# Kernel tuning notes

Measured on AMD Instinct MI355X. Metric: run time of the kernel, lower is better.

## Reference

```python
import jax, jax.numpy as jnp
import numpy as np
import math

B, T, C = 4, 2048, 768
H = 12
D = C // H  # head dim 64

def setup_inputs() -> dict:
    key = jax.random.key(0)
    ks = jax.random.split(key, 7)
    hidden_states = jax.random.normal(ks[0], (B, T, C), dtype=jnp.float32)
    attention_mask = jnp.ones((B, T), dtype=jnp.float32)
    # torch nn.Linear weights are [out, in]; y = x @ W.T + b
    s = 1.0 / math.sqrt(C)
    Wq = jax.random.uniform(ks[1], (C, C), jnp.float32, -s, s)
    bq = jax.random.uniform(ks[2], (C,), jnp.float32, -s, s)
    Wk = jax.random.uniform(ks[3], (C, C), jnp.float32, -s, s)
    bk = jax.random.uniform(ks[4], (C,), jnp.float32, -s, s)
    Wv = jax.random.uniform(ks[5], (C, C), jnp.float32, -s, s)
    bv = jax.random.uniform(ks[6], (C,), jnp.float32, -s, s)
    return {"hidden_states": hidden_states, "attention_mask": attention_mask,
            "Wq": Wq, "bq": bq, "Wk": Wk, "bk": bk, "Wv": Wv, "bv": bv}

def _split_heads(x):
    # [B,T,C] -> [B,H,T,D]
    b, t, c = x.shape
    return x.reshape(b, t, H, D).transpose(0, 2, 1, 3)

def reference(hidden_states, attention_mask, Wq, bq, Wk, bk, Wv, bv):
    q = _split_heads(hidden_states @ Wq.T + bq)
    k = _split_heads(hidden_states @ Wk.T + bk)
    v = _split_heads(hidden_states @ Wv.T + bv)
    scores = jnp.einsum("bhqd,bhkd->bhqk", q, k) / jnp.sqrt(jnp.float32(D))
    # mask: [B,T] -> additive bias [B,1,1,T]
    bias = (1.0 - attention_mask)[:, None, None, :] * -10000.0
    scores = scores + bias
    probs = jax.nn.softmax(scores, axis=-1)  # dropout prob = 0 -> identity
    ctx = jnp.einsum("bhqk,bhkd->bhqd", probs, v)
    # [B,H,T,D] -> [B,T,C]
    return ctx.transpose(0, 2, 1, 3).reshape(hidden_states.shape[0], hidden_states.shape[1], C)
```

## Files before the change

### kernel.cpp

```cpp
#include <hip/hip_runtime.h>
#include <hip/hip_bf16.h>
#include <cstdint>

#define DI __device__ __forceinline__

constexpr int Bz = 4, Tz = 2048, Cz = 768, Hz = 12, Dz = 64;
constexpr float QSCALE = 0.18033688011112042f;

typedef __attribute__((ext_vector_type(4))) float f32x4;
typedef __attribute__((ext_vector_type(16))) float f32x16;
typedef __attribute__((ext_vector_type(8))) __bf16 bf16x8;
typedef __attribute__((ext_vector_type(4))) __bf16 bf16x4;
typedef __attribute__((ext_vector_type(2))) __bf16 bf16x2;

typedef __attribute__((address_space(1))) void gvoid;
typedef __attribute__((address_space(3))) void lvoid;

DI void gload16(const void* g, void* l) {
  __builtin_amdgcn_global_load_lds((gvoid*)g, (lvoid*)l, 16, 0, 0);
}

DI f32x4 mfma16(bf16x8 a, bf16x8 b, f32x4 c) {
  return __builtin_amdgcn_mfma_f32_16x16x32_bf16(a, b, c, 0, 0, 0);
}
DI f32x16 mfma32(bf16x8 a, bf16x8 b, f32x16 c) {
  return __builtin_amdgcn_mfma_f32_32x32x16_bf16(a, b, c, 0, 0, 0);
}

DI uint32_t pk2(float a, float b) {
  bf16x2 t;
  t[0] = (__bf16)a;
  t[1] = (__bf16)b;
  return __builtin_bit_cast(uint32_t, t);
}

union FragU { bf16x8 v; uint32_t u[4]; };

__global__ void cvt_f32_bf16_k(const float* __restrict__ src,
                               __bf16* __restrict__ dst, int n4) {
  int i = blockIdx.x * blockDim.x + threadIdx.x;
  if (i >= n4) return;
  const float4 v = reinterpret_cast<const float4*>(src)[i];
  bf16x4 r = {(__bf16)v.x, (__bf16)v.y, (__bf16)v.z, (__bf16)v.w};
  reinterpret_cast<bf16x4*>(dst)[i] = r;
}

__global__ void cvt_w3_k(const float* __restrict__ wq, const float* __restrict__ wk,
                         const float* __restrict__ wv, __bf16* __restrict__ dst) {
  int i = blockIdx.x * blockDim.x + threadIdx.x;
  const int which = i / 147456;
  const int r = i - which * 147456;
  const float* s = (which == 0) ? wq : (which == 1) ? wk : wv;
  const float4 v = reinterpret_cast<const float4*>(s)[r];
  bf16x4 o = {(__bf16)v.x, (__bf16)v.y, (__bf16)v.z, (__bf16)v.w};
  reinterpret_cast<bf16x4*>(dst)[i] = o;
}

__global__ __launch_bounds__(256, 4) void qkv_gemm_k(
    const __bf16* __restrict__ Xb, const __bf16* __restrict__ Wb,
    const float* __restrict__ bq, const float* __restrict__ bk,
    const float* __restrict__ bv, __bf16* __restrict__ Qo,
    __bf16* __restrict__ Ko, __bf16* __restrict__ Vo) {
  __shared__ __align__(16) __bf16 As[128 * 64];
  __shared__ __align__(16) __bf16 Bs[128 * 64];

  const int tid = threadIdx.x;
  const int lane = tid & 63;
  const int w = tid >> 6;
  const int wr = w >> 1, wc = w & 1;
  const int g = lane >> 4, lr = lane & 15;

  const int wgid = (blockIdx.x & 7) * 144 + (blockIdx.x >> 3);
  const int tn = wgid % 18, tm = wgid / 18;
  const int m0 = tm * 128, n0 = tn * 128;

  f32x4 acc[4][4] = {};

  for (int kt = 0; kt < Cz; kt += 64) {
#pragma unroll
    for (int rep = 0; rep < 4; ++rep) {
      const int c = rep * 256 + tid;
      const int row = c >> 3, blk = c & 7;
      const int col = ((blk ^ (row & 7)) << 3);
      gload16(&Xb[(size_t)(m0 + row) * Cz + kt + col], &As[c << 3]);
      gload16(&Wb[(size_t)(n0 + row) * Cz + kt + col], &Bs[c << 3]);
    }
    __syncthreads();
#pragma unroll
    for (int kk = 0; kk < 2; ++kk) {
      bf16x8 a[4], b[4];
#pragma unroll
      for (int m = 0; m < 4; ++m) {
        const int row = wr * 64 + m * 16 + lr;
        a[m] = *reinterpret_cast<const bf16x8*>(
            &As[row * 64 + (((kk * 4 + g) ^ (row & 7)) << 3)]);
      }
#pragma unroll
      for (int n = 0; n < 4; ++n) {
        const int row = wc * 64 + n * 16 + lr;
        b[n] = *reinterpret_cast<const bf16x8*>(
            &Bs[row * 64 + (((kk * 4 + g) ^ (row & 7)) << 3)]);
      }
      __builtin_amdgcn_s_setprio(1);
#pragma unroll
      for (int m = 0; m < 4; ++m)
#pragma unroll
        for (int n = 0; n < 4; ++n) acc[m][n] = mfma16(a[m], b[n], acc[m][n]);
      __builtin_amdgcn_s_setprio(0);
    }
    __syncthreads();
  }

#pragma unroll
  for (int n = 0; n < 4; ++n) {
    const int gn = n0 + wc * 64 + n * 16 + lr;
    const int which = gn / Cz;
    const int cc = gn - which * Cz;
    const int h = cc >> 6, d = cc & 63;
    const float* bsrc = (which == 0) ? bq : (which == 1) ? bk : bv;
    const float bsv = bsrc[cc];
    __bf16* dst = (which == 0) ? Qo : (which == 1) ? Ko : Vo;
#pragma unroll
    for (int m = 0; m < 4; ++m) {
#pragma unroll
      for (int j = 0; j < 4; ++j) {
        const int gm = m0 + wr * 64 + m * 16 + g * 4 + j;
        const int bb = gm >> 11, t = gm & 2047;
        const int bh = bb * Hz + h;
        float v = acc[m][n][j] + bsv;
        if (which == 0) v *= QSCALE;
        const size_t idx = (which == 2) ? ((size_t)(bh * Dz + d) * Tz + t)
                                        : ((size_t)(bh * Tz + t) * Dz + d);
        dst[idx] = (__bf16)v;
      }
    }
  }
}

__global__ __launch_bounds__(256, 3) void attn_k(
    const __bf16* __restrict__ Qg, const __bf16* __restrict__ Kg,
    const __bf16* __restrict__ Vg, const float* __restrict__ mask,
    float* __restrict__ out) {
  __shared__ __align__(16) __bf16 Ks[2][4096];
  __shared__ __align__(16) __bf16 Vs[2][4096];

  const int tid = threadIdx.x;
  const int lane = tid & 63;
  const int w = tid >> 6;
  const int hi = lane >> 5;
  const int l31 = lane & 31;

  const int wg = (blockIdx.x & 7) * 96 + (blockIdx.x >> 3);
  const int bh = wg >> 4, qt = wg & 15;
  const int bb = bh / Hz, h = bh - bb * Hz;
  const int q0 = qt * 128 + w * 32;

  const size_t qkbase = (size_t)bh * Tz * Dz;
  const size_t vbase = (size_t)bh * Dz * Tz;
  const float* maskp = &mask[bb * Tz];

  int* flag = (int*)&Ks[1][0];
  if (tid == 0) *flag = 0;
  __syncthreads();
  {
    int mybad = 0;
    for (int i = tid; i < Tz; i += 256) mybad |= (maskp[i] != 1.0f);
    if (__any(mybad) && lane == 0) atomicOr(flag, 1);
  }

#pragma unroll
  for (int rep = 0; rep < 2; ++rep) {
    const int c = rep * 256 + tid;
    const int row = c >> 3, blk = c & 7;
    const int col = ((blk ^ (row & 7)) << 3);
    gload16(&Kg[qkbase + (size_t)row * Dz + col], &Ks[0][c << 3]);
    gload16(&Vg[vbase + (size_t)row * Tz + col], &Vs[0][c << 3]);
  }

  bf16x8 qB[4];
#pragma unroll
  for (int ks = 0; ks < 4; ++ks)
    qB[ks] = *reinterpret_cast<const bf16x8*>(
        &Qg[qkbase + (size_t)(q0 + l31) * Dz + ks * 16 + hi * 8]);

  __syncthreads();
  const bool use_mask = (*flag != 0);

  int rOff[4];
#pragma unroll
  for (int i = 0; i < 4; ++i)
    rOff[i] = l31 * 64 + (((i * 2 + hi) ^ (l31 & 7)) << 3);

  f32x16 o0 = {}, o1 = {};
  float lpart = 0.f;

  for (int t2 = 0; t2 < 16; ++t2) {
#pragma unroll
    for (int sub = 0; sub < 2; ++sub) {
      const int t = 2 * t2 + sub;
      __syncthreads();
      if (t < 31) {
        const int kt1 = (t + 1) * 64;
#pragma unroll
        for (int rep = 0; rep < 2; ++rep) {
          const int c = rep * 256 + tid;
          const int row = c >> 3, blk = c & 7;
          const int col = ((blk ^ (row & 7)) << 3);
          gload16(&Kg[qkbase + (size_t)(kt1 + row) * Dz + col],
                  &Ks[sub ^ 1][c << 3]);
          gload16(&Vg[vbase + (size_t)row * Tz + kt1 + col],
                  &Vs[sub ^ 1][c << 3]);
        }
      }
      const int kt = t * 64;

#pragma unroll
      for (int kblk = 0; kblk < 2; ++kblk) {
        bf16x8 kA[4], vB0[2], vB1[2];
#pragma unroll
        for (int ks = 0; ks < 4; ++ks)
          kA[ks] = *reinterpret_cast<const bf16x8*>(
              &Ks[sub][kblk * 2048 + rOff[ks]]);
#pragma unroll
        for (int pss = 0; pss < 2; ++pss) {
          vB0[pss] = *reinterpret_cast<const bf16x8*>(
              &Vs[sub][rOff[kblk * 2 + pss]]);
          vB1[pss] = *reinterpret_cast<const bf16x8*>(
              &Vs[sub][2048 + rOff[kblk * 2 + pss]]);
        }

        f32x16 s = {};
        __builtin_amdgcn_s_setprio(1);
#pragma unroll
        for (int ks = 0; ks < 4; ++ks) s = mfma32(kA[ks], qB[ks], s);
        __builtin_amdgcn_s_setprio(0);

        float p[16];
        if (use_mask) {
#pragma unroll
          for (int r = 0; r < 16; ++r) {
            const int kg = kt + kblk * 32 + (r & 3) + 8 * (r >> 2) + 4 * hi;
            p[r] = __builtin_amdgcn_exp2f(
                s[r] + (1.0f - maskp[kg]) * -14426.950408889634f);
            lpart += p[r];
          }
        } else {
#pragma unroll
          for (int r = 0; r < 16; ++r) {
            p[r] = __builtin_amdgcn_exp2f(s[r]);
            lpart += p[r];
          }
        }

        uint32_t a0 = pk2(p[0], p[1]), a1 = pk2(p[4], p[5]);
        uint32_t a2 = pk2(p[8], p[9]), a3 = pk2(p[12], p[13]);
        uint32_t b0 = pk2(p[2], p[3]), b1 = pk2(p[6], p[7]);
        uint32_t b2 = pk2(p[10], p[11]), b3 = pk2(p[14], p[15]);
        asm volatile("v_permlane32_swap_b32 %0, %1" : "+v"(a0), "+v"(a1));
        asm volatile("v_permlane32_swap_b32 %0, %1" : "+v"(b0), "+v"(b1));
        asm volatile("v_permlane32_swap_b32 %0, %1" : "+v"(a2), "+v"(a3));
        asm volatile("v_permlane32_swap_b32 %0, %1" : "+v"(b2), "+v"(b3));
        FragU pf0, pf1;
        pf0.u[0] = a0; pf0.u[1] = b0; pf0.u[2] = a1; pf0.u[3] = b1;
        pf1.u[0] = a2; pf1.u[1] = b2; pf1.u[2] = a3; pf1.u[3] = b3;

        __builtin_amdgcn_s_setprio(1);
        o0 = mfma32(pf0.v, vB0[0], o0);
        o1 = mfma32(pf0.v, vB1[0], o1);
        o0 = mfma32(pf1.v, vB0[1], o0);
        o1 = mfma32(pf1.v, vB1[1], o1);
        __builtin_amdgcn_s_setprio(0);
      }
    }
  }

  float lfin = lpart + __shfl_xor(lpart, 32);
  const float inv = 1.0f / lfin;
#pragma unroll
  for (int r = 0; r < 16; ++r) {
    const int qr = (r & 3) + 8 * (r >> 2) + 4 * hi;
    const float invr = __shfl(inv, qr);
    float* orow = &out[(size_t)(bb * Tz + q0 + qr) * Cz + h * Dz + l31];
    orow[0] = o0[r] * invr;
    orow[32] = o1[r] * invr;
  }
}

extern "C" void kernel_launch(void* const* d_in, const int* in_sizes, int n_in,
                              void* d_out, int out_size, void* d_ws,
                              size_t ws_size, hipStream_t stream) {
  const float* x = (const float*)d_in[0];
  const float* mask = (const float*)d_in[1];
  const float* Wq = (const float*)d_in[2];
  const float* bq = (const float*)d_in[3];
  const float* Wk = (const float*)d_in[4];
  const float* bk = (const float*)d_in[5];
  const float* Wv = (const float*)d_in[6];
  const float* bv = (const float*)d_in[7];
  float* out = (float*)d_out;

  char* ws = (char*)d_ws;
  __bf16* Xb = (__bf16*)ws;
  __bf16* Wb = (__bf16*)(ws + 12582912);
  __bf16* Qb = (__bf16*)(ws + 16131072);
  __bf16* Kb = (__bf16*)(ws + 16131072 + 12582912);
  __bf16* Vb = (__bf16*)(ws + 16131072 + 2 * 12582912);

  cvt_f32_bf16_k<<<6144, 256, 0, stream>>>(x, Xb, 1572864);
  cvt_w3_k<<<1728, 256, 0, stream>>>(Wq, Wk, Wv, Wb);
  qkv_gemm_k<<<1152, 256, 0, stream>>>(Xb, Wb, bq, bk, bv, Qb, Kb, Vb);
  attn_k<<<768, 256, 0, stream>>>(Qb, Kb, Vb, mask, out);
}
```

Baseline: 135.5 us.

## Store V in MFMA-fragment layout and load it directly into registers

The QKV GEMM epilogue now writes V in a chunked layout that matches the MFMA B-fragment order, using packed 4-element stores. The attention kernel then reads V fragments straight from global memory into registers, with no LDS staging, and drops the V shared-memory buffers. This is meant to cut LDS traffic and footprint and to vectorize the V stores. The two conversion kernels are also merged into one launch. In exchange, V loads are now synchronous global reads at the top of each tile, which may expose latency because there is no prefetch. The converter also keeps a dead duplicate assignment.

```diff
diff --git a/kernel.cpp b/kernel.cpp
--- a/kernel.cpp
+++ b/kernel.cpp
@@ -36,24 +36,27 @@
 
 union FragU { bf16x8 v; uint32_t u[4]; };
 
-__global__ void cvt_f32_bf16_k(const float* __restrict__ src,
-                               __bf16* __restrict__ dst, int n4) {
+__global__ void cvt_all_k(const float* __restrict__ x,
+                          const float* __restrict__ wq, const float* __restrict__ wk,
+                          const float* __restrict__ wv, __bf16* __restrict__ Xb,
+                          __bf16* __restrict__ Wb) {
   int i = blockIdx.x * blockDim.x + threadIdx.x;
-  if (i >= n4) return;
-  const float4 v = reinterpret_cast<const float4*>(src)[i];
-  bf16x4 r = {(__bf16)v.x, (__bf16)v.y, (__bf16)v.z, (__bf16)v.w};
-  reinterpret_cast<bf16x4*>(dst)[i] = r;
-}
-
-__global__ void cvt_w3_k(const float* __restrict__ wq, const float* __restrict__ wk,
-                         const float* __restrict__ wv, __bf16* __restrict__ dst) {
-  int i = blockIdx.x * blockDim.x + threadIdx.x;
-  const int which = i / 147456;
-  const int r = i - which * 147456;
-  const float* s = (which == 0) ? wq : (which == 1) ? wk : wv;
+  const float* s;
+  __bf16* d;
+  int r;
+  if (i < 1572864) {
+    s = x; d = Xb; r = i;
+  } else {
+    int j = i - 1572864;
+    const int which = j / 147456;
+    r = j - which * 147456;
+    s = (which == 0) ? wq : (which == 1) ? wk : wv;
+    d = Wb + which * 589824 * 2;
+    d = Wb + which * 589824;
+  }
   const float4 v = reinterpret_cast<const float4*>(s)[r];
   bf16x4 o = {(__bf16)v.x, (__bf16)v.y, (__bf16)v.z, (__bf16)v.w};
-  reinterpret_cast<bf16x4*>(dst)[i] = o;
+  reinterpret_cast<bf16x4*>(d)[r] = o;
 }
 
 __global__ __launch_bounds__(256, 4) void qkv_gemm_k(
@@ -111,27 +114,45 @@
     __syncthreads();
   }
 
-#pragma unroll
-  for (int n = 0; n < 4; ++n) {
-    const int gn = n0 + wc * 64 + n * 16 + lr;
-    const int which = gn / Cz;
-    const int cc = gn - which * Cz;
-    const int h = cc >> 6, d = cc & 63;
-    const float* bsrc = (which == 0) ? bq : (which == 1) ? bk : bv;
-    const float bsv = bsrc[cc];
-    __bf16* dst = (which == 0) ? Qo : (which == 1) ? Ko : Vo;
-#pragma unroll
-    for (int m = 0; m < 4; ++m) {
-#pragma unroll
-      for (int j = 0; j < 4; ++j) {
-        const int gm = m0 + wr * 64 + m * 16 + g * 4 + j;
-        const int bb = gm >> 11, t = gm & 2047;
-        const int bh = bb * Hz + h;
-        float v = acc[m][n][j] + bsv;
-        if (which == 0) v *= QSCALE;
-        const size_t idx = (which == 2) ? ((size_t)(bh * Dz + d) * Tz + t)
-                                        : ((size_t)(bh * Tz + t) * Dz + d);
-        dst[idx] = (__bf16)v;
+  const int bb = m0 >> 11;
+  const int tbase = m0 & 2047;
+  if (tn >= 12) {
+#pragma unroll
+    for (int n = 0; n < 4; ++n) {
+      const int cc = (n0 - 1536) + wc * 64 + n * 16 + lr;
+      const int h = cc >> 6, d = cc & 63;
+      const float bsv = bv[cc];
+      const int bh = bb * Hz + h;
+#pragma unroll
+      for (int m = 0; m < 4; ++m) {
+        const int tloc = tbase + wr * 64 + m * 16 + g * 4;
+        const int k16 = tloc >> 4;
+        bf16x4 pkv;
+#pragma unroll
+        for (int j = 0; j < 4; ++j) pkv[j] = (__bf16)(acc[m][n][j] + bsv);
+        *reinterpret_cast<bf16x4*>(
+            &Vo[((size_t)(bh * 128 + k16) * 64 + d) * 16 + (tloc & 15)]) = pkv;
+      }
+    }
+  } else {
+    const bool isQ = (tn < 6);
+#pragma unroll
+    for (int n = 0; n < 4; ++n) {
+      const int gn = n0 + wc * 64 + n * 16 + lr;
+      const int cc = isQ ? gn : (gn - 768);
+      const int h = cc >> 6, d = cc & 63;
+      const float bsv = isQ ? bq[cc] : bk[cc];
+      __bf16* dst = isQ ? Qo : Ko;
+      const int bh = bb * Hz + h;
+#pragma unroll
+      for (int m = 0; m < 4; ++m) {
+#pragma unroll
+        for (int j = 0; j < 4; ++j) {
+          const int t = tbase + wr * 64 + m * 16 + g * 4 + j;
+          float v = acc[m][n][j] + bsv;
+          if (isQ) v *= QSCALE;
+          dst[(size_t)(bh * Tz + t) * Dz + d] = (__bf16)v;
+        }
       }
     }
   }
@@ -139,10 +160,9 @@
 
 __global__ __launch_bounds__(256, 3) void attn_k(
     const __bf16* __restrict__ Qg, const __bf16* __restrict__ Kg,
-    const __bf16* __restrict__ Vg, const float* __restrict__ mask,
+    const __bf16* __restrict__ Vc, const float* __restrict__ mask,
     float* __restrict__ out) {
   __shared__ __align__(16) __bf16 Ks[2][4096];
-  __shared__ __align__(16) __bf16 Vs[2][4096];
 
   const int tid = threadIdx.x;
   const int lane = tid & 63;
@@ -156,7 +176,7 @@
   const int q0 = qt * 128 + w * 32;
 
   const size_t qkbase = (size_t)bh * Tz * Dz;
-  const size_t vbase = (size_t)bh * Dz * Tz;
+  const size_t vcb = (size_t)bh * Tz * Dz;
   const float* maskp = &mask[bb * Tz];
 
   int* flag = (int*)&Ks[1][0];
@@ -174,7 +194,6 @@
     const int row = c >> 3, blk = c & 7;
     const int col = ((blk ^ (row & 7)) << 3);
     gload16(&Kg[qkbase + (size_t)row * Dz + col], &Ks[0][c << 3]);
-    gload16(&Vg[vbase + (size_t)row * Tz + col], &Vs[0][c << 3]);
   }
 
   bf16x8 qB[4];
@@ -186,10 +205,12 @@
   __syncthreads();
   const bool use_mask = (*flag != 0);
 
-  int rOff[4];
+  int off4[4];
 #pragma unroll
   for (int i = 0; i < 4; ++i)
-    rOff[i] = l31 * 64 + (((i * 2 + hi) ^ (l31 & 7)) << 3);
+    off4[i] = l31 * 64 + (((i * 2 + hi) ^ (l31 & 7)) << 3);
+
+  const int vlane0 = l31 * 16 + hi * 8;
 
   f32x16 o0 = {}, o1 = {};
   float lpart = 0.f;
@@ -199,6 +220,15 @@
     for (int sub = 0; sub < 2; ++sub) {
       const int t = 2 * t2 + sub;
       __syncthreads();
+
+      bf16x8 vB[4][2];
+#pragma unroll
+      for (int ps4 = 0; ps4 < 4; ++ps4) {
+        const size_t cb = vcb + (size_t)(t * 4 + ps4) * 1024;
+        vB[ps4][0] = *reinterpret_cast<const bf16x8*>(&Vc[cb + vlane0]);
+        vB[ps4][1] = *reinterpret_cast<const bf16x8*>(&Vc[cb + 512 + vlane0]);
+      }
+
       if (t < 31) {
         const int kt1 = (t + 1) * 64;
 #pragma unroll
@@ -208,26 +238,17 @@
           const int col = ((blk ^ (row & 7)) << 3);
           gload16(&Kg[qkbase + (size_t)(kt1 + row) * Dz + col],
                   &Ks[sub ^ 1][c << 3]);
-          gload16(&Vg[vbase + (size_t)row * Tz + kt1 + col],
-                  &Vs[sub ^ 1][c << 3]);
         }
       }
       const int kt = t * 64;
 
 #pragma unroll
       for (int kblk = 0; kblk < 2; ++kblk) {
-        bf16x8 kA[4], vB0[2], vB1[2];
+        bf16x8 kA[4];
 #pragma unroll
         for (int ks = 0; ks < 4; ++ks)
           kA[ks] = *reinterpret_cast<const bf16x8*>(
-              &Ks[sub][kblk * 2048 + rOff[ks]]);
-#pragma unroll
-        for (int pss = 0; pss < 2; ++pss) {
-          vB0[pss] = *reinterpret_cast<const bf16x8*>(
-              &Vs[sub][rOff[kblk * 2 + pss]]);
-          vB1[pss] = *reinterpret_cast<const bf16x8*>(
-              &Vs[sub][2048 + rOff[kblk * 2 + pss]]);
-        }
+              &Ks[sub][kblk * 2048 + off4[ks]]);
 
         f32x16 s = {};
         __builtin_amdgcn_s_setprio(1);
@@ -265,10 +286,10 @@
         pf1.u[0] = a2; pf1.u[1] = b2; pf1.u[2] = a3; pf1.u[3] = b3;
 
         __builtin_amdgcn_s_setprio(1);
-        o0 = mfma32(pf0.v, vB0[0], o0);
-        o1 = mfma32(pf0.v, vB1[0], o1);
-        o0 = mfma32(pf1.v, vB0[1], o0);
-        o1 = mfma32(pf1.v, vB1[1], o1);
+        o0 = mfma32(pf0.v, vB[kblk * 2][0], o0);
+        o1 = mfma32(pf0.v, vB[kblk * 2][1], o1);
+        o0 = mfma32(pf1.v, vB[kblk * 2 + 1][0], o0);
+        o1 = mfma32(pf1.v, vB[kblk * 2 + 1][1], o1);
         __builtin_amdgcn_s_setprio(0);
       }
     }
@@ -306,8 +327,7 @@
   __bf16* Kb = (__bf16*)(ws + 16131072 + 12582912);
   __bf16* Vb = (__bf16*)(ws + 16131072 + 2 * 12582912);
 
-  cvt_f32_bf16_k<<<6144, 256, 0, stream>>>(x, Xb, 1572864);
-  cvt_w3_k<<<1728, 256, 0, stream>>>(Wq, Wk, Wv, Wb);
+  cvt_all_k<<<7872, 256, 0, stream>>>(x, Wq, Wk, Wv, Xb, Wb);
   qkv_gemm_k<<<1152, 256, 0, stream>>>(Xb, Wb, bq, bk, bv, Qb, Kb, Vb);
   attn_k<<<768, 256, 0, stream>>>(Qb, Kb, Vb, mask, out);
 }
```

After: 116.4 us. -14.1%, faster.
